# Performance work log

Hardware: AMD Instinct MI355X
Metric: run time of the kernel (lower is better)

## Reference

```python
import jax, jax.numpy as jnp
import numpy as np

B, L, D = 2, 512, 1024
INNER = 32
PAIR = 128


def setup_inputs() -> dict:
    key = jax.random.key(0)
    ks = jax.random.split(key, 6)
    scale = lambda fan_in: 1.0 / np.sqrt(fan_in)
    return {
        "sequence_state": jax.random.normal(ks[0], (B, L, D), dtype=jnp.float32),
        "ln_gamma": jnp.ones((D,), dtype=jnp.float32),
        "ln_beta": jnp.zeros((D,), dtype=jnp.float32),
        "W_proj": jax.random.normal(ks[1], (2 * INNER, D), dtype=jnp.float32) * scale(D),
        "b_proj": jnp.zeros((2 * INNER,), dtype=jnp.float32),
        "W_o": jax.random.normal(ks[2], (PAIR, 2 * INNER), dtype=jnp.float32) * scale(2 * INNER),
        "b_o": jnp.zeros((PAIR,), dtype=jnp.float32),
    }


def reference(sequence_state, ln_gamma, ln_beta, W_proj, b_proj, W_o, b_o):
    eps = 1e-5
    # LayerNorm over last dim
    mu = jnp.mean(sequence_state, axis=-1, keepdims=True)
    var = jnp.mean(jnp.square(sequence_state - mu), axis=-1, keepdims=True)
    s = (sequence_state - mu) * jax.lax.rsqrt(var + eps) * ln_gamma + ln_beta
    # proj: B x L x 2*inner
    s = jnp.einsum("bld,ed->ble", s, W_proj) + b_proj
    q, k = jnp.split(s, 2, axis=-1)  # each B x L x inner
    # broadcast outer product / difference: B x L x L x inner
    prod = q[:, None, :, :] * k[:, :, None, :]
    diff = q[:, None, :, :] - k[:, :, None, :]
    x = jnp.concatenate([prod, diff], axis=-1)  # B x L x L x 2*inner
    # o_proj: B x L x L x pairwise
    x = jnp.einsum("bije,pe->bijp", x, W_o) + b_o
    return x
```

## Files before the change

kernel.cpp:

```cpp
#include <hip/hip_runtime.h>
#include <hip/hip_bf16.h>
#include <stdint.h>


typedef __attribute__((ext_vector_type(8))) short short8;
typedef __attribute__((ext_vector_type(4))) float floatx4;

__device__ __forceinline__ unsigned short f2bf(float f) {
    union { float f; unsigned int u; } v; v.f = f;
    return (unsigned short)((v.u + 0x7FFFu + ((v.u >> 16) & 1u)) >> 16);
}

__global__ __launch_bounds__(256) void k0_transpose(
    const float* __restrict__ Wproj, const float* __restrict__ Wo,
    float* __restrict__ Wt, float* __restrict__ Wot, float* __restrict__ Wdt)
{
    int g = blockIdx.x * 256 + threadIdx.x;
    if (g < 65536) {
        int o = g >> 10, d = g & 1023;
        Wt[d * 64 + o] = Wproj[g];
    } else {
        int h = g - 65536;
        int p = h & 127, e = h >> 7;
        float v = Wo[p * 64 + e];
        if (e < 32) Wot[e * 128 + p] = v;
        else        Wdt[(e - 32) * 128 + p] = v;
    }
}

__global__ __launch_bounds__(256) void k1_ln_proj(
    const float* __restrict__ x, const float* __restrict__ gamma, const float* __restrict__ beta,
    const float* __restrict__ Wt, const float* __restrict__ b_proj,
    const float* __restrict__ Wdt, const float* __restrict__ b_o,
    unsigned short* __restrict__ Qbf, float* __restrict__ Kf, float* __restrict__ C0)
{
    __shared__ float s_sh[4][1024];
    __shared__ float part[4][64][5];
    __shared__ float k_sh[4][32];

    const int t = threadIdx.x;
    const int w = t >> 6;
    const int lane = t & 63;
    const int row = blockIdx.x * 4 + w;

    const float* xr = x + (size_t)row * 1024;
    floatx4 xv[4];
    float sum = 0.f, sq = 0.f;
#pragma unroll
    for (int c = 0; c < 4; ++c) {
        xv[c] = *(const floatx4*)(xr + (c * 64 + lane) * 4);
        sum += xv[c].x + xv[c].y + xv[c].z + xv[c].w;
        sq  += xv[c].x * xv[c].x + xv[c].y * xv[c].y + xv[c].z * xv[c].z + xv[c].w * xv[c].w;
    }
#pragma unroll
    for (int m = 1; m < 64; m <<= 1) {
        sum += __shfl_xor(sum, m, 64);
        sq  += __shfl_xor(sq,  m, 64);
    }
    const float mu   = sum * (1.f / 1024.f);
    const float var  = sq * (1.f / 1024.f) - mu * mu;
    const float rsig = rsqrtf(var + 1e-5f);
#pragma unroll
    for (int c = 0; c < 4; ++c) {
        int d = (c * 64 + lane) * 4;
        floatx4 g4 = *(const floatx4*)(gamma + d);
        floatx4 b4 = *(const floatx4*)(beta + d);
        floatx4 s4;
        s4.x = (xv[c].x - mu) * rsig * g4.x + b4.x;
        s4.y = (xv[c].y - mu) * rsig * g4.y + b4.y;
        s4.z = (xv[c].z - mu) * rsig * g4.z + b4.z;
        s4.w = (xv[c].w - mu) * rsig * g4.w + b4.w;
        *(floatx4*)(&s_sh[w][d]) = s4;
    }
    __syncthreads();

    {
        const int o = t & 63;
        const int ch = t >> 6;
        float a0 = 0.f, a1 = 0.f, a2 = 0.f, a3 = 0.f;
        const float* wp = Wt + (size_t)ch * 256 * 64 + o;
#pragma unroll 4
        for (int d = 0; d < 256; ++d) {
            float wv = wp[(size_t)d * 64];
            int dd = ch * 256 + d;
            a0 += s_sh[0][dd] * wv;
            a1 += s_sh[1][dd] * wv;
            a2 += s_sh[2][dd] * wv;
            a3 += s_sh[3][dd] * wv;
        }
        part[0][o][ch] = a0; part[1][o][ch] = a1;
        part[2][o][ch] = a2; part[3][o][ch] = a3;
    }
    __syncthreads();

    {
        const int r = t >> 6, oo = t & 63;
        float v = part[r][oo][0] + part[r][oo][1] + part[r][oo][2] + part[r][oo][3] + b_proj[oo];
        const int rowr = blockIdx.x * 4 + r;
        if (oo < 32) {
            Qbf[rowr * 32 + oo] = f2bf(v);
        } else {
            Kf[rowr * 32 + (oo - 32)] = v;
            k_sh[r][oo - 32] = v;
        }
    }
    __syncthreads();

    {
        const int p = t & 127;
        const int r0 = t >> 7;
#pragma unroll
        for (int rr = 0; rr < 2; ++rr) {
            const int r = r0 * 2 + rr;
            float a = 0.f;
#pragma unroll 8
            for (int e = 0; e < 32; ++e) a += k_sh[r][e] * Wdt[e * 128 + p];
            C0[(size_t)(blockIdx.x * 4 + r) * 128 + p] = b_o[p] - a;
        }
    }
}

__global__ __launch_bounds__(256) void k2_pair(
    const unsigned short* __restrict__ Qbf, const float* __restrict__ Kf,
    const float* __restrict__ C0, const float* __restrict__ Wot, const float* __restrict__ Wdt,
    float* __restrict__ out)
{
    __shared__ unsigned short G[32 * 136];
    __shared__ float c0s[128];
    __shared__ float ksh[32];

    const int t  = threadIdx.x;
    const int bi = blockIdx.x;
    const int b  = bi >> 9;

    if (t < 32)  ksh[t]  = Kf[(size_t)bi * 32 + t];
    if (t < 128) c0s[t] = C0[(size_t)bi * 128 + t];
    __syncthreads();

#pragma unroll
    for (int it = 0; it < 16; ++it) {
        int idx = it * 256 + t;
        int e = idx >> 7, p = idx & 127;
        float gv = ksh[e] * Wot[idx] + Wdt[idx];
        G[e * 136 + p] = f2bf(gv);
    }
    __syncthreads();

    const int wave = t >> 6, lane = t & 63;
    const int col = lane & 15, quad = lane >> 4;

    short8 bfrag[8];
#pragma unroll
    for (int pt = 0; pt < 8; ++pt) {
        short8 f;
#pragma unroll
        for (int u = 0; u < 8; ++u)
            f[u] = (short)G[(quad * 8 + u) * 136 + pt * 16 + col];
        bfrag[pt] = f;
    }
    float cv[8];
#pragma unroll
    for (int pt = 0; pt < 8; ++pt) cv[pt] = c0s[pt * 16 + col];

    const size_t outbase = (size_t)bi * (512 * 128);

    for (int l = 0; l < 8; ++l) {
        const int jt = wave * 8 + l;
        const int j0 = jt * 16;
        const short8 afrag =
            *(const short8*)(Qbf + ((size_t)b * 512 + j0 + col) * 32 + quad * 8);
        floatx4 acc[8];
#pragma unroll
        for (int pt = 0; pt < 8; ++pt) {
            floatx4 c;
            c.x = cv[pt]; c.y = cv[pt]; c.z = cv[pt]; c.w = cv[pt];
            acc[pt] = __builtin_amdgcn_mfma_f32_16x16x32_bf16(afrag, bfrag[pt], c, 0, 0, 0);
        }
        float* op = out + outbase + (size_t)(j0 + quad * 4) * 128 + col;
#pragma unroll
        for (int pt = 0; pt < 8; ++pt) {
#pragma unroll
            for (int r = 0; r < 4; ++r) {
                op[r * 128 + pt * 16] = acc[pt][r];
            }
        }
    }
}

extern "C" void kernel_launch(void* const* d_in, const int* in_sizes, int n_in,
                              void* d_out, int out_size, void* d_ws, size_t ws_size,
                              hipStream_t stream) {
    const float* x     = (const float*)d_in[0];
    const float* gamma = (const float*)d_in[1];
    const float* beta  = (const float*)d_in[2];
    const float* Wproj = (const float*)d_in[3];
    const float* bproj = (const float*)d_in[4];
    const float* Wo    = (const float*)d_in[5];
    const float* bo    = (const float*)d_in[6];
    float* out = (float*)d_out;

    float* ws = (float*)d_ws;
    float* Wt  = ws;
    float* Wot = ws + 65536;
    float* Wdt = ws + 69632;
    float* Kf  = ws + 73728;
    float* C0  = ws + 106496;
    unsigned short* Qbf = (unsigned short*)(ws + 237568);

    hipLaunchKernelGGL(k0_transpose, dim3(288), dim3(256), 0, stream,
                       Wproj, Wo, Wt, Wot, Wdt);
    hipLaunchKernelGGL(k1_ln_proj, dim3(256), dim3(256), 0, stream,
                       x, gamma, beta, Wt, bproj, Wdt, bo, Qbf, Kf, C0);
    hipLaunchKernelGGL(k2_pair, dim3(1024), dim3(256), 0, stream,
                       Qbf, Kf, C0, Wot, Wdt, out);
}
```

Measured before the change: 293.9 us.

## Stage pair-kernel output through LDS for coalesced nontemporal float4 stores

The pair kernel now writes each MFMA tile into a per-wave LDS buffer and reads it back as contiguous float4 rows, which are written to global memory with nontemporal stores. This replaces the strided scalar stores. The grid is doubled so each block handles half of the j range, adding parallelism at the cost of recomputing G per half. The projection GEMM in k1 is also vectorized to float4 weight loads with a 16-way split over d. These changes target the 134MB output write, which dominates runtime, and add extra LDS traffic and shared memory use.

```diff
diff --git a/kernel.cpp b/kernel.cpp
--- a/kernel.cpp
+++ b/kernel.cpp
@@ -9,6 +9,10 @@
 __device__ __forceinline__ unsigned short f2bf(float f) {
     union { float f; unsigned int u; } v; v.f = f;
     return (unsigned short)((v.u + 0x7FFFu + ((v.u >> 16) & 1u)) >> 16);
+}
+
+__device__ __forceinline__ floatx4 fmadd4(float s, floatx4 w, floatx4 a) {
+    a.x += s * w.x; a.y += s * w.y; a.z += s * w.z; a.w += s * w.w; return a;
 }
 
 __global__ __launch_bounds__(256) void k0_transpose(
@@ -34,8 +38,8 @@
     const float* __restrict__ Wdt, const float* __restrict__ b_o,
     unsigned short* __restrict__ Qbf, float* __restrict__ Kf, float* __restrict__ C0)
 {
-    __shared__ float s_sh[4][1024];
-    __shared__ float part[4][64][5];
+    __shared__ __attribute__((aligned(16))) float s_sh[4][1024];
+    __shared__ __attribute__((aligned(16))) float part[4][16][68];
     __shared__ float k_sh[4][32];
 
     const int t = threadIdx.x;
@@ -75,27 +79,32 @@
     __syncthreads();
 
     {
-        const int o = t & 63;
-        const int ch = t >> 6;
-        float a0 = 0.f, a1 = 0.f, a2 = 0.f, a3 = 0.f;
-        const float* wp = Wt + (size_t)ch * 256 * 64 + o;
-#pragma unroll 4
-        for (int d = 0; d < 256; ++d) {
-            float wv = wp[(size_t)d * 64];
-            int dd = ch * 256 + d;
-            a0 += s_sh[0][dd] * wv;
-            a1 += s_sh[1][dd] * wv;
-            a2 += s_sh[2][dd] * wv;
-            a3 += s_sh[3][dd] * wv;
-        }
-        part[0][o][ch] = a0; part[1][o][ch] = a1;
-        part[2][o][ch] = a2; part[3][o][ch] = a3;
+        const int o4 = t & 15;
+        const int ch = t >> 4;
+        const floatx4* Wt4 = (const floatx4*)Wt;
+        floatx4 a0 = {0.f, 0.f, 0.f, 0.f}, a1 = a0, a2 = a0, a3 = a0;
+        const int dbase = ch * 64;
+#pragma unroll 8
+        for (int dd = 0; dd < 64; ++dd) {
+            const int d = dbase + dd;
+            floatx4 w4 = Wt4[d * 16 + o4];
+            a0 = fmadd4(s_sh[0][d], w4, a0);
+            a1 = fmadd4(s_sh[1][d], w4, a1);
+            a2 = fmadd4(s_sh[2][d], w4, a2);
+            a3 = fmadd4(s_sh[3][d], w4, a3);
+        }
+        *(floatx4*)&part[0][ch][o4 * 4] = a0;
+        *(floatx4*)&part[1][ch][o4 * 4] = a1;
+        *(floatx4*)&part[2][ch][o4 * 4] = a2;
+        *(floatx4*)&part[3][ch][o4 * 4] = a3;
     }
     __syncthreads();
 
     {
         const int r = t >> 6, oo = t & 63;
-        float v = part[r][oo][0] + part[r][oo][1] + part[r][oo][2] + part[r][oo][3] + b_proj[oo];
+        float v = b_proj[oo];
+#pragma unroll
+        for (int c = 0; c < 16; ++c) v += part[r][c][oo];
         const int rowr = blockIdx.x * 4 + r;
         if (oo < 32) {
             Qbf[rowr * 32 + oo] = f2bf(v);
@@ -126,14 +135,16 @@
     float* __restrict__ out)
 {
     __shared__ unsigned short G[32 * 136];
+    __shared__ __attribute__((aligned(16))) float T[4][16][132];
     __shared__ float c0s[128];
     __shared__ float ksh[32];
 
-    const int t  = threadIdx.x;
-    const int bi = blockIdx.x;
-    const int b  = bi >> 9;
-
-    if (t < 32)  ksh[t]  = Kf[(size_t)bi * 32 + t];
+    const int t    = threadIdx.x;
+    const int bi   = blockIdx.x >> 1;
+    const int half = blockIdx.x & 1;
+    const int b    = bi >> 9;
+
+    if (t < 32)  ksh[t] = Kf[(size_t)bi * 32 + t];
     if (t < 128) c0s[t] = C0[(size_t)bi * 128 + t];
     __syncthreads();
 
@@ -163,9 +174,10 @@
     for (int pt = 0; pt < 8; ++pt) cv[pt] = c0s[pt * 16 + col];
 
     const size_t outbase = (size_t)bi * (512 * 128);
-
-    for (int l = 0; l < 8; ++l) {
-        const int jt = wave * 8 + l;
+    float (*Tw)[132] = T[wave];
+
+    for (int l = 0; l < 4; ++l) {
+        const int jt = half * 16 + wave * 4 + l;
         const int j0 = jt * 16;
         const short8 afrag =
             *(const short8*)(Qbf + ((size_t)b * 512 + j0 + col) * 32 + quad * 8);
@@ -176,13 +188,19 @@
             c.x = cv[pt]; c.y = cv[pt]; c.z = cv[pt]; c.w = cv[pt];
             acc[pt] = __builtin_amdgcn_mfma_f32_16x16x32_bf16(afrag, bfrag[pt], c, 0, 0, 0);
         }
-        float* op = out + outbase + (size_t)(j0 + quad * 4) * 128 + col;
 #pragma unroll
         for (int pt = 0; pt < 8; ++pt) {
 #pragma unroll
-            for (int r = 0; r < 4; ++r) {
-                op[r * 128 + pt * 16] = acc[pt][r];
-            }
+            for (int r = 0; r < 4; ++r)
+                Tw[quad * 4 + r][pt * 16 + col] = acc[pt][r];
+        }
+        float* orow = out + outbase + (size_t)j0 * 128;
+#pragma unroll
+        for (int s = 0; s < 8; ++s) {
+            int idx = s * 64 + lane;
+            int rr = idx >> 5, c4 = idx & 31;
+            floatx4 v = *(const floatx4*)&Tw[rr][c4 * 4];
+            __builtin_nontemporal_store(v, (floatx4*)(orow + rr * 128 + c4 * 4));
         }
     }
 }
@@ -211,6 +229,6 @@
                        Wproj, Wo, Wt, Wot, Wdt);
     hipLaunchKernelGGL(k1_ln_proj, dim3(256), dim3(256), 0, stream,
                        x, gamma, beta, Wt, bproj, Wdt, bo, Qbf, Kf, C0);
-    hipLaunchKernelGGL(k2_pair, dim3(1024), dim3(256), 0, stream,
+    hipLaunchKernelGGL(k2_pair, dim3(2048), dim3(256), 0, stream,
                        Qbf, Kf, C0, Wot, Wdt, out);
 }
```

Result: faster. 284.8 us (-3.1%).
